# Kernel tuning notes

Hardware: AMD Instinct MI355X
Metric: run time of the kernel (lower is better)

The kernel has to match this reference:

```python
import jax, jax.numpy as jnp
from jax import lax
import numpy as np

ALPHA = 1.0
GAMMA = 1e-6
KBLK = 64  # codebook block size for the L1 NN search scan


def setup_inputs() -> dict:
    key = jax.random.key(0)
    ks = jax.random.split(key, 6)
    B, T, C, F, D, K = 8, 1024, 32, 256, 128, 512
    return {
        "X": jax.random.normal(ks[0], (B, T, C), jnp.float32),
        "H": jax.random.normal(ks[1], (B, D, T), jnp.float32),
        "M": jax.random.normal(ks[2], (D, K), jnp.float32),
        "Hdec": jax.random.normal(ks[3], (B, T, F), jnp.float32),
        "W": jax.random.normal(ks[4], (C, F), jnp.float32) * 0.05,
        "w_d": jax.random.normal(ks[5], (C,), jnp.float32) * 0.05,
    }


def _memory_loss(H, M):
    # H: [B, D, T], M: [D, K]
    Ht = jnp.transpose(H, (0, 2, 1))            # [B, T, D]
    MT = M.T                                     # [K, D] codewords
    K, D = MT.shape
    nblk = K // KBLK
    blocks = MT.reshape(nblk, KBLK, D)
    bases = jnp.arange(nblk, dtype=jnp.int32) * KBLK

    def step(carry, blk_base):
        best_d, best_i = carry
        blk, base = blk_base
        # L1 distance to this block of codewords: [B, T, KBLK]
        d = jnp.sum(jnp.abs(Ht[:, :, None, :] - blk[None, None, :, :]), axis=-1)
        bd = jnp.min(d, axis=-1)
        bi = jnp.argmin(d, axis=-1).astype(jnp.int32) + base
        upd = bd < best_d  # strict < keeps the first (lowest-index) argmin, as torch does
        return (jnp.where(upd, bd, best_d), jnp.where(upd, bi, best_i)), None

    init = (jnp.full(Ht.shape[:2], jnp.inf, Ht.dtype),
            jnp.zeros(Ht.shape[:2], jnp.int32))
    (_, best_i), _ = lax.scan(step, init, (blocks, bases))

    Zt = MT[best_i]  # [B, T, D] gathered nearest codewords
    sg = lax.stop_gradient
    # sum of per-(b,d) squared L2 norms over T == total squared sum
    diffs = jnp.sum((sg(Ht) - Zt) ** 2) + jnp.sum((Ht - sg(Zt)) ** 2)
    return diffs / float(np.prod(H.shape))


def reference(X, H, M, Hdec, W, w_d):
    # decoder last layer + discriminator head (needed for adaptive weight grads)
    def rec_loss(w):
        Xhat = jnp.einsum('btf,cf->btc', Hdec, w)
        return jnp.mean((Xhat - X) ** 2)

    def d_loss(w):
        Xhat = jnp.einsum('btf,cf->btc', Hdec, w)
        return -jnp.mean(Xhat @ w_d)

    loss_rec = rec_loss(W)
    loss_d = d_loss(W)
    loss_m = _memory_loss(H, M)

    g_rec = jax.grad(rec_loss)(W)
    g_d = jax.grad(d_loss)(W)
    lmbda = lax.stop_gradient(
        jnp.linalg.norm(g_rec) / (jnp.linalg.norm(g_d) + GAMMA))

    return loss_rec + ALPHA * loss_m + lmbda * loss_d
```

## Files before the change

kernel.cpp:

```cpp
#include <hip/hip_runtime.h>
#include <hip/hip_bf16.h>
#include <math.h>

#define N_POS 8192
#define D_DIM 128
#define K_DIM 512
#define C_DIM 32
#define F_DIM 256
#define NKT   4
#define GREC_COLS 8448
#define L2_BLOCKS 388
#define NN_BLOCKS 512

__device__ __forceinline__ float block_reduce_256(float v) {
    __shared__ float sbuf[4];
    __syncthreads();
#pragma unroll
    for (int off = 32; off > 0; off >>= 1) v += __shfl_down(v, off);
    const int lane = threadIdx.x & 63;
    const int w    = threadIdx.x >> 6;
    if (lane == 0) sbuf[w] = v;
    __syncthreads();
    return (threadIdx.x == 0) ? (sbuf[0] + sbuf[1] + sbuf[2] + sbuf[3]) : 0.f;
}

__global__ __launch_bounds__(256)
void fused_l1(const float* __restrict__ H, const float* __restrict__ M,
              const float* __restrict__ Hdec, const float* __restrict__ W,
              const float* __restrict__ X, const float* __restrict__ w_d,
              float* __restrict__ MT, float* __restrict__ pd,
              int* __restrict__ pi, float* __restrict__ pp,
              float* __restrict__ accum) {
    __shared__ __align__(16) char smem_raw[38912];
    const int tid = threadIdx.x;

    if (blockIdx.x < NN_BLOCKS) {
        float* hT = (float*)smem_raw;
        float* mT = hT + 2048;
        float* rd = hT;
        int*   ri = (int*)(hT + 1024);

        const int ptile = blockIdx.x >> 2;
        const int ktile = blockIdx.x & 3;
        const int pos0  = ptile << 6;
        const int b     = pos0 >> 10;
        const int t0    = pos0 & 1023;
        const int k0    = ktile << 7;
        const float* Hb = H + (b << 17) + t0;

        const int hq = (tid & 15) << 2;
        const int hr = tid >> 4;
        const int mq = (tid & 31) << 2;
        const int mr = tid >> 5;
        const int p4 = (tid & 15) << 2;
        const int q4 = (tid >> 4) << 2;

        float acc[4][8];
#pragma unroll
        for (int i = 0; i < 4; ++i)
#pragma unroll
            for (int j = 0; j < 8; ++j) acc[i][j] = 0.f;

        auto absacc32 = [&](const float4& A,
                            const float4& Ma, const float4& Mc) {
            const float hh[4] = {A.x,  A.y,  A.z,  A.w};
            const float mm[8] = {Ma.x, Ma.y, Ma.z, Ma.w, Mc.x, Mc.y, Mc.z, Mc.w};
#pragma unroll
            for (int i = 0; i < 4; ++i)
#pragma unroll
                for (int j = 0; j < 8; ++j) {
                    const float dv = hh[i] - mm[j];
                    asm("v_add_f32 %0, %0, abs(%1)"
                        : "+v"(acc[i][j]) : "v"(dv));
                }
        };

        const float* hrow = hT + p4;
        const float* mrow = mT + q4;

        for (int ch = 0; ch < 4; ++ch) {
            const int d0 = ch << 5;
            __syncthreads();
#pragma unroll
            for (int p = 0; p < 2; ++p) {
                const int d = (p << 4) + hr;
                *(float4*)(hT + (d << 6) + hq) =
                    *(const float4*)(Hb + ((size_t)(d0 + d) << 10) + hq);
            }
#pragma unroll
            for (int p = 0; p < 4; ++p) {
                const int d = (p << 3) + mr;
                *(float4*)(mT + (d << 7) + mq) =
                    *(const float4*)(M + (size_t)(d0 + d) * K_DIM + k0 + mq);
            }
            __syncthreads();

            float4 ha = *(const float4*)(hrow);
            float4 ma = *(const float4*)(mrow);
            float4 mc = *(const float4*)(mrow + 64);
#pragma unroll 2
            for (int d = 0; d < 31; ++d) {
                const float4 nha = *(const float4*)(hrow + ((d + 1) << 6));
                const float4 nma = *(const float4*)(mrow + ((d + 1) << 7));
                const float4 nmc = *(const float4*)(mrow + ((d + 1) << 7) + 64);
                absacc32(ha, ma, mc);
                ha = nha; ma = nma; mc = nmc;
            }
            absacc32(ha, ma, mc);
        }

        __syncthreads();

#pragma unroll
        for (int i = 0; i < 4; ++i) {
            const int pl = p4 + i;
            float bd = acc[i][0];
            int   bj = 0;
#pragma unroll
            for (int j = 1; j < 8; ++j)
                if (acc[i][j] < bd) { bd = acc[i][j]; bj = j; }
            const int bk = k0 + ((bj < 4) ? (q4 + bj) : (64 + q4 + bj - 4));
            rd[(tid >> 4) * 64 + pl] = bd;
            ri[(tid >> 4) * 64 + pl] = bk;
        }
        __syncthreads();

        if (tid < 64) {
            float bd = rd[tid];
            int   bi = ri[tid];
#pragma unroll
            for (int q = 1; q < 16; ++q) {
                const float d = rd[q * 64 + tid];
                const int   k = ri[q * 64 + tid];
                if (d < bd || (d == bd && k < bi)) { bd = d; bi = k; }
            }
            pd[ktile * N_POS + pos0 + tid] = bd;
            pi[ktile * N_POS + pos0 + tid] = bi;
        }
    } else {
        float* Wl = (float*)smem_raw;
        float* El = Wl + C_DIM * 260;
        const int xb  = blockIdx.x - NN_BLOCKS;
        const int bt0 = xb << 5;

        if (xb < 64) {
            const int d0 = xb << 1;
            const int d  = d0 + (tid >> 7);
            const int k  = (tid & 127) << 2;
#pragma unroll
            for (int j = 0; j < 4; ++j)
                MT[(size_t)(k + j) * D_DIM + d] = M[(size_t)d * K_DIM + k + j];
        }

#pragma unroll
        for (int it = 0; it < 8; ++it) {
            const int i = it * 1024 + tid * 4;
            const float4 v = *(const float4*)(W + i);
            *(float4*)(Wl + (i >> 8) * 260 + (i & 255)) = v;
        }
        __syncthreads();

        const int c  = tid & 31;
        const int rg = tid >> 5;
        const int r0 = bt0 + rg, r1 = r0 + 8, r2 = r0 + 16, r3 = r0 + 24;

        float a0 = 0.f, a1 = 0.f, a2 = 0.f, a3 = 0.f;
#pragma unroll 4
        for (int f0 = 0; f0 < F_DIM; f0 += 4) {
            const float4 w4 = *(const float4*)(Wl + c * 260 + f0);
            const float4 h0 = *(const float4*)(Hdec + (size_t)r0 * F_DIM + f0);
            const float4 h1 = *(const float4*)(Hdec + (size_t)r1 * F_DIM + f0);
            const float4 h2 = *(const float4*)(Hdec + (size_t)r2 * F_DIM + f0);
            const float4 h3 = *(const float4*)(Hdec + (size_t)r3 * F_DIM + f0);
            a0 += h0.x * w4.x + h0.y * w4.y + h0.z * w4.z + h0.w * w4.w;
            a1 += h1.x * w4.x + h1.y * w4.y + h1.z * w4.z + h1.w * w4.w;
            a2 += h2.x * w4.x + h2.y * w4.y + h2.z * w4.z + h2.w * w4.w;
            a3 += h3.x * w4.x + h3.y * w4.y + h3.z * w4.z + h3.w * w4.w;
        }

        const float wd = w_d[c];
        const float e0 = a0 - X[(size_t)r0 * C_DIM + c];
        const float e1 = a1 - X[(size_t)r1 * C_DIM + c];
        const float e2 = a2 - X[(size_t)r2 * C_DIM + c];
        const float e3 = a3 - X[(size_t)r3 * C_DIM + c];
        El[(rg)      * 32 + c] = e0;
        El[(rg + 8)  * 32 + c] = e1;
        El[(rg + 16) * 32 + c] = e2;
        El[(rg + 24) * 32 + c] = e3;
        const float sse = e0 * e0 + e1 * e1 + e2 * e2 + e3 * e3;
        const float dp  = (a0 + a1 + a2 + a3) * wd;
        const float rA = block_reduce_256(sse);
        if (tid == 0) atomicAdd(accum + 0, rA);
        const float rB = block_reduce_256(dp);
        if (tid == 0) atomicAdd(accum + 1, rB);
        __syncthreads();

        const int f = tid;
        float gacc[C_DIM];
#pragma unroll
        for (int cc = 0; cc < C_DIM; ++cc) gacc[cc] = 0.f;
        float sf = 0.f;
#pragma unroll 1
        for (int i = 0; i < 32; ++i) {
            const float hd = Hdec[(size_t)(bt0 + i) * F_DIM + f];
            sf += hd;
#pragma unroll
            for (int c4 = 0; c4 < 8; ++c4) {
                const float4 e4 = *(const float4*)(El + i * 32 + c4 * 4);
                gacc[c4 * 4 + 0] += e4.x * hd;
                gacc[c4 * 4 + 1] += e4.y * hd;
                gacc[c4 * 4 + 2] += e4.z * hd;
                gacc[c4 * 4 + 3] += e4.w * hd;
            }
        }
        float* o = pp + (size_t)xb * GREC_COLS;
#pragma unroll
        for (int cc = 0; cc < C_DIM; ++cc) o[cc * F_DIM + f] = gacc[cc];
        o[8192 + f] = sf;
    }
}

__global__ __launch_bounds__(256)
void fused_l2(const float* __restrict__ H, const float* __restrict__ MT,
              const float* __restrict__ pd, const int* __restrict__ pi,
              const float* __restrict__ pp, const float* __restrict__ w_d,
              float* __restrict__ accum, float* __restrict__ out) {
    const int tid = threadIdx.x;
    if (blockIdx.x < 256) {
        const int bx = blockIdx.x & 31;
        const int by = blockIdx.x >> 5;
        const int pos = bx * 256 + tid;
        const int b = pos >> 10;
        const int t = pos & 1023;

        float bd = INFINITY;
        int   bi = 0x7fffffff;
#pragma unroll
        for (int p = 0; p < NKT; ++p) {
            const float d = pd[p * N_POS + pos];
            const int   k = pi[p * N_POS + pos];
            if (d < bd || (d == bd && k < bi)) { bd = d; bi = k; }
        }

        const int d0 = by * 16;
        const float* Hb = H + (b << 17) + t + (d0 << 10);
        const float* z  = MT + (size_t)bi * D_DIM + d0;
        const float4 z0 = *(const float4*)(z);
        const float4 z1 = *(const float4*)(z + 4);
        const float4 z2 = *(const float4*)(z + 8);
        const float4 z3 = *(const float4*)(z + 12);
        float s0 = 0.f, s1 = 0.f, s2 = 0.f, s3 = 0.f;
        float e;
        e = Hb[0  << 10] - z0.x; s0 += e * e;
        e = Hb[1  << 10] - z0.y; s1 += e * e;
        e = Hb[2  << 10] - z0.z; s2 += e * e;
        e = Hb[3  << 10] - z0.w; s3 += e * e;
        e = Hb[4  << 10] - z1.x; s0 += e * e;
        e = Hb[5  << 10] - z1.y; s1 += e * e;
        e = Hb[6  << 10] - z1.z; s2 += e * e;
        e = Hb[7  << 10] - z1.w; s3 += e * e;
        e = Hb[8  << 10] - z2.x; s0 += e * e;
        e = Hb[9  << 10] - z2.y; s1 += e * e;
        e = Hb[10 << 10] - z2.z; s2 += e * e;
        e = Hb[11 << 10] - z2.w; s3 += e * e;
        e = Hb[12 << 10] - z3.x; s0 += e * e;
        e = Hb[13 << 10] - z3.y; s1 += e * e;
        e = Hb[14 << 10] - z3.z; s2 += e * e;
        e = Hb[15 << 10] - z3.w; s3 += e * e;
        const float r = block_reduce_256((s0 + s1) + (s2 + s3));
        if (tid == 0) atomicAdd(accum + 2, r);
    } else {
        const int g = blockIdx.x - 256;
        const int col = (g < 128) ? (g * 64 + (tid & 63))
                                  : (8192 + (g - 128) * 64 + (tid & 63));
        const int pc  = tid >> 6;
        const float* base = pp + (size_t)(pc * 64) * GREC_COLS + col;
        float s = 0.f;
#pragma unroll 8
        for (int p = 0; p < 64; ++p) s += base[(size_t)p * GREC_COLS];
        __shared__ float red[4][64];
        red[pc][tid & 63] = s;
        __syncthreads();
        if (tid < 64) {
            const float tot = red[0][tid] + red[1][tid] +
                              red[2][tid] + red[3][tid];
            float v = tot * tot;
#pragma unroll
            for (int off = 32; off > 0; off >>= 1) v += __shfl_down(v, off);
            if (tid == 0)
                atomicAdd(accum + ((g >= 128) ? 4 : 3), v);
        }
    }

    __shared__ int is_last;
    if (tid == 0) {
        __threadfence();
        unsigned int* cnt = (unsigned int*)(accum + 5);
        is_last = (atomicAdd(cnt, 1u) == L2_BLOCKS - 1);
    }
    __syncthreads();
    if (is_last && tid < 64) {
        float wd2 = (tid < C_DIM) ? w_d[tid] * w_d[tid] : 0.f;
#pragma unroll
        for (int off = 32; off > 0; off >>= 1) wd2 += __shfl_down(wd2, off);
        if (tid == 0) {
            __threadfence();
            const float sse_rec = atomicAdd(accum + 0, 0.f);
            const float dsum    = atomicAdd(accum + 1, 0.f);
            const float sse_mem = atomicAdd(accum + 2, 0.f);
            const float g2      = atomicAdd(accum + 3, 0.f);
            const float s2      = atomicAdd(accum + 4, 0.f);
            const float loss_rec = sse_rec / 262144.f;
            const float loss_d   = -dsum / 8192.f;
            const float loss_m   = 2.f * sse_mem / 1048576.f;
            const float ngrec    = (2.f / 262144.f) * sqrtf(g2);
            const float ngd      = sqrtf(wd2 * s2) / 8192.f;
            const float lmbda    = ngrec / (ngd + 1e-6f);
            out[0] = loss_rec + loss_m + lmbda * loss_d;
        }
    }
}

extern "C" void kernel_launch(void* const* d_in, const int* in_sizes, int n_in,
                              void* d_out, int out_size, void* d_ws, size_t ws_size,
                              hipStream_t stream) {
    const float* X    = (const float*)d_in[0];
    const float* H    = (const float*)d_in[1];
    const float* M    = (const float*)d_in[2];
    const float* Hdec = (const float*)d_in[3];
    const float* W    = (const float*)d_in[4];
    const float* w_d  = (const float*)d_in[5];

    float* ws    = (float*)d_ws;
    float* MT    = ws;
    float* accum = ws + 65536;
    float* pd    = ws + 65552;
    int*   pi    = (int*)(ws + 98320);
    float* pp    = ws + 131088;

    hipMemsetAsync(accum, 0, 16 * sizeof(float), stream);
    fused_l1<<<768,       256, 0, stream>>>(H, M, Hdec, W, X, w_d,
                                            MT, pd, pi, pp, accum);
    fused_l2<<<L2_BLOCKS, 256, 0, stream>>>(H, MT, pd, pi, pp, w_d,
                                            accum, (float*)d_out);
}
```

Before: 132.0 us.

## Prefetch NN tiles into registers, reorder blocks, and hoist loads ahead of dependencies

The L1 nearest-neighbour blocks now load the next 32-row chunk of H and M into registers while computing on the current shared-memory chunk. This double-buffers global loads across the compute loop. The gradient blocks are moved to the front of the grid so they start first. The Hdec loop prefetches two rows ahead, and fused_l2 issues its H loads before the dependent argmin merge so their latency overlaps. These changes add register pressure, which may lower occupancy.

```diff
diff --git a/kernel.cpp b/kernel.cpp
--- a/kernel.cpp
+++ b/kernel.cpp
@@ -34,26 +34,46 @@
     __shared__ __align__(16) char smem_raw[38912];
     const int tid = threadIdx.x;
 
-    if (blockIdx.x < NN_BLOCKS) {
+    if (blockIdx.x >= 256) {
         float* hT = (float*)smem_raw;
         float* mT = hT + 2048;
         float* rd = hT;
         int*   ri = (int*)(hT + 1024);
 
-        const int ptile = blockIdx.x >> 2;
-        const int ktile = blockIdx.x & 3;
+        const int nb    = blockIdx.x - 256;
+        const int ptile = nb >> 2;
+        const int ktile = nb & 3;
         const int pos0  = ptile << 6;
         const int b     = pos0 >> 10;
         const int t0    = pos0 & 1023;
         const int k0    = ktile << 7;
         const float* Hb = H + (b << 17) + t0;
 
-        const int hq = (tid & 15) << 2;
-        const int hr = tid >> 4;
-        const int mq = (tid & 31) << 2;
-        const int mr = tid >> 5;
         const int p4 = (tid & 15) << 2;
         const int q4 = (tid >> 4) << 2;
+
+        const float* hsrc = Hb + (size_t)(tid >> 4) * 1024 + ((tid & 15) << 2);
+        const float* msrc = M  + (size_t)(tid >> 5) * K_DIM + k0 + ((tid & 31) << 2);
+        float* hdst = hT + (tid << 2);
+        float* mdst = mT + (tid << 2);
+
+        float4 rh[2][2], rm[2][4];
+#define LDCH(P, CH) do {                                                      \
+        rh[P][0] = *(const float4*)(hsrc + (size_t)((CH)*32 +  0) * 1024);    \
+        rh[P][1] = *(const float4*)(hsrc + (size_t)((CH)*32 + 16) * 1024);    \
+        rm[P][0] = *(const float4*)(msrc + (size_t)((CH)*32 +  0) * 512);     \
+        rm[P][1] = *(const float4*)(msrc + (size_t)((CH)*32 +  8) * 512);     \
+        rm[P][2] = *(const float4*)(msrc + (size_t)((CH)*32 + 16) * 512);     \
+        rm[P][3] = *(const float4*)(msrc + (size_t)((CH)*32 + 24) * 512);     \
+    } while (0)
+#define STCH(P) do {                                                          \
+        *(float4*)(hdst)        = rh[P][0];                                   \
+        *(float4*)(hdst + 1024) = rh[P][1];                                   \
+        *(float4*)(mdst)        = rm[P][0];                                   \
+        *(float4*)(mdst + 1024) = rm[P][1];                                   \
+        *(float4*)(mdst + 2048) = rm[P][2];                                   \
+        *(float4*)(mdst + 3072) = rm[P][3];                                   \
+    } while (0)
 
         float acc[4][8];
 #pragma unroll
@@ -78,22 +98,15 @@
         const float* hrow = hT + p4;
         const float* mrow = mT + q4;
 
+        LDCH(0, 0);
+#pragma unroll
         for (int ch = 0; ch < 4; ++ch) {
-            const int d0 = ch << 5;
             __syncthreads();
-#pragma unroll
-            for (int p = 0; p < 2; ++p) {
-                const int d = (p << 4) + hr;
-                *(float4*)(hT + (d << 6) + hq) =
-                    *(const float4*)(Hb + ((size_t)(d0 + d) << 10) + hq);
-            }
-#pragma unroll
-            for (int p = 0; p < 4; ++p) {
-                const int d = (p << 3) + mr;
-                *(float4*)(mT + (d << 7) + mq) =
-                    *(const float4*)(M + (size_t)(d0 + d) * K_DIM + k0 + mq);
-            }
+            if (ch & 1) STCH(1); else STCH(0);
             __syncthreads();
+            if (ch == 0) LDCH(1, 1);
+            else if (ch == 1) LDCH(0, 2);
+            else if (ch == 2) LDCH(1, 3);
 
             float4 ha = *(const float4*)(hrow);
             float4 ma = *(const float4*)(mrow);
@@ -108,6 +121,8 @@
             }
             absacc32(ha, ma, mc);
         }
+#undef LDCH
+#undef STCH
 
         __syncthreads();
 
@@ -140,7 +155,7 @@
     } else {
         float* Wl = (float*)smem_raw;
         float* El = Wl + C_DIM * 260;
-        const int xb  = blockIdx.x - NN_BLOCKS;
+        const int xb  = blockIdx.x;
         const int bt0 = xb << 5;
 
         if (xb < 64) {
@@ -196,22 +211,39 @@
         __syncthreads();
 
         const int f = tid;
+        const float* hp = Hdec + (size_t)bt0 * F_DIM + f;
         float gacc[C_DIM];
 #pragma unroll
         for (int cc = 0; cc < C_DIM; ++cc) gacc[cc] = 0.f;
         float sf = 0.f;
+        float hd0 = hp[0];
+        float hd1 = hp[F_DIM];
 #pragma unroll 1
-        for (int i = 0; i < 32; ++i) {
-            const float hd = Hdec[(size_t)(bt0 + i) * F_DIM + f];
-            sf += hd;
+        for (int i = 0; i < 30; ++i) {
+            const float hdn = hp[(size_t)(i + 2) * F_DIM];
+            sf += hd0;
 #pragma unroll
             for (int c4 = 0; c4 < 8; ++c4) {
                 const float4 e4 = *(const float4*)(El + i * 32 + c4 * 4);
-                gacc[c4 * 4 + 0] += e4.x * hd;
-                gacc[c4 * 4 + 1] += e4.y * hd;
-                gacc[c4 * 4 + 2] += e4.z * hd;
-                gacc[c4 * 4 + 3] += e4.w * hd;
+                gacc[c4 * 4 + 0] += e4.x * hd0;
+                gacc[c4 * 4 + 1] += e4.y * hd0;
+                gacc[c4 * 4 + 2] += e4.z * hd0;
+                gacc[c4 * 4 + 3] += e4.w * hd0;
             }
+            hd0 = hd1; hd1 = hdn;
+        }
+#pragma unroll
+        for (int i = 30; i < 32; ++i) {
+            sf += hd0;
+#pragma unroll
+            for (int c4 = 0; c4 < 8; ++c4) {
+                const float4 e4 = *(const float4*)(El + i * 32 + c4 * 4);
+                gacc[c4 * 4 + 0] += e4.x * hd0;
+                gacc[c4 * 4 + 1] += e4.y * hd0;
+                gacc[c4 * 4 + 2] += e4.z * hd0;
+                gacc[c4 * 4 + 3] += e4.w * hd0;
+            }
+            hd0 = hd1;
         }
         float* o = pp + (size_t)xb * GREC_COLS;
 #pragma unroll
@@ -233,6 +265,12 @@
         const int b = pos >> 10;
         const int t = pos & 1023;
 
+        const int d0 = by * 16;
+        const float* Hb = H + (b << 17) + t + (d0 << 10);
+        float hv[16];
+#pragma unroll
+        for (int j = 0; j < 16; ++j) hv[j] = Hb[j << 10];
+
         float bd = INFINITY;
         int   bi = 0x7fffffff;
 #pragma unroll
@@ -242,8 +280,6 @@
             if (d < bd || (d == bd && k < bi)) { bd = d; bi = k; }
         }
 
-        const int d0 = by * 16;
-        const float* Hb = H + (b << 17) + t + (d0 << 10);
         const float* z  = MT + (size_t)bi * D_DIM + d0;
         const float4 z0 = *(const float4*)(z);
         const float4 z1 = *(const float4*)(z + 4);
@@ -251,22 +287,22 @@
         const float4 z3 = *(const float4*)(z + 12);
         float s0 = 0.f, s1 = 0.f, s2 = 0.f, s3 = 0.f;
         float e;
-        e = Hb[0  << 10] - z0.x; s0 += e * e;
-        e = Hb[1  << 10] - z0.y; s1 += e * e;
-        e = Hb[2  << 10] - z0.z; s2 += e * e;
-        e = Hb[3  << 10] - z0.w; s3 += e * e;
-        e = Hb[4  << 10] - z1.x; s0 += e * e;
-        e = Hb[5  << 10] - z1.y; s1 += e * e;
-        e = Hb[6  << 10] - z1.z; s2 += e * e;
-        e = Hb[7  << 10] - z1.w; s3 += e * e;
-        e = Hb[8  << 10] - z2.x; s0 += e * e;
-        e = Hb[9  << 10] - z2.y; s1 += e * e;
-        e = Hb[10 << 10] - z2.z; s2 += e * e;
-        e = Hb[11 << 10] - z2.w; s3 += e * e;
-        e = Hb[12 << 10] - z3.x; s0 += e * e;
-        e = Hb[13 << 10] - z3.y; s1 += e * e;
-        e = Hb[14 << 10] - z3.z; s2 += e * e;
-        e = Hb[15 << 10] - z3.w; s3 += e * e;
+        e = hv[0]  - z0.x; s0 += e * e;
+        e = hv[1]  - z0.y; s1 += e * e;
+        e = hv[2]  - z0.z; s2 += e * e;
+        e = hv[3]  - z0.w; s3 += e * e;
+        e = hv[4]  - z1.x; s0 += e * e;
+        e = hv[5]  - z1.y; s1 += e * e;
+        e = hv[6]  - z1.z; s2 += e * e;
+        e = hv[7]  - z1.w; s3 += e * e;
+        e = hv[8]  - z2.x; s0 += e * e;
+        e = hv[9]  - z2.y; s1 += e * e;
+        e = hv[10] - z2.z; s2 += e * e;
+        e = hv[11] - z2.w; s3 += e * e;
+        e = hv[12] - z3.x; s0 += e * e;
+        e = hv[13] - z3.y; s1 += e * e;
+        e = hv[14] - z3.z; s2 += e * e;
+        e = hv[15] - z3.w; s3 += e * e;
         const float r = block_reduce_256((s0 + s1) + (s2 + s3));
         if (tid == 0) atomicAdd(accum + 2, r);
     } else {
```

Result: no change. 133.6 us (+1.2%).
